# Kernel optimization log

Measured on AMD Instinct MI355X. Metric: run time of the kernel, lower is better.

The kernel has to match this reference:

```python
import jax, jax.numpy as jnp
import numpy as np


def setup_inputs() -> dict:
    key = jax.random.key(0)
    k1, k2, k3 = jax.random.split(key, 3)
    inp = jax.random.normal(k1, (32, 128, 56, 56), dtype=jnp.float32)
    # kaiming-style scale for a 3x3 conv kernel
    fan_in = 128 * 3 * 3
    kernel = jax.random.normal(k2, (256, 128, 3, 3), dtype=jnp.float32) * np.float32(np.sqrt(2.0 / fan_in))
    bias = jax.random.normal(k3, (256,), dtype=jnp.float32)
    return {"inp": inp, "kernel": kernel, "bias": bias}


def reference(inp, kernel, bias):
    # 3x3 conv, stride 1, padding 1 (SAME), NCHW / OIHW layout, plus bias.
    out = jax.lax.conv_general_dilated(
        inp, kernel,
        window_strides=(1, 1),
        padding=((1, 1), (1, 1)),
        dimension_numbers=("NCHW", "OIHW", "NCHW"),
    )
    return out + bias[None, :, None, None]
```

## Files before the change

### kernel.cpp

```cpp
#include <hip/hip_runtime.h>
#include <hip/hip_bf16.h>


#define C_IN   128
#define K_OUT  256
#define HW     56
#define IMG    3136
#define NBATCH 32
#define PW     58
#define KTOT   1152
#define IN_WS_USHORT ((size_t)4*NBATCH*PW*256*8)
#define WT_WS_USHORT ((size_t)12*2*1536*8)

typedef __bf16 bf16x8 __attribute__((ext_vector_type(8)));
typedef float  f32x4  __attribute__((ext_vector_type(4)));
typedef unsigned short ushort8 __attribute__((ext_vector_type(8)));

__device__ inline unsigned short f2bf(float f) {
    unsigned int u = __builtin_bit_cast(unsigned int, f);
    u += ((u >> 16) & 1u) + 0x7FFFu;
    return (unsigned short)(u >> 16);
}

__device__ __forceinline__ void gl2lds16(const unsigned short* g, unsigned short* l) {
    __builtin_amdgcn_global_load_lds(
        (const __attribute__((address_space(1))) unsigned int*)g,
        (__attribute__((address_space(3))) unsigned int*)l, 16, 0, 0);
}

__global__ void prep_input(const float* __restrict__ inp,
                           unsigned short* __restrict__ dst) {
    __shared__ unsigned short tile[C_IN * 57];
    int n = blockIdx.x / PW, py = blockIdx.x % PW;
    ushort8* d8 = (ushort8*)dst;
    const bool border = (py == 0 || py == PW - 1);
    if (!border) {
        const float* src = inp + (size_t)n * C_IN * IMG + (py - 1) * HW;
        for (int i = threadIdx.x; i < C_IN * HW; i += 256) {
            int c = i / HW, x = i - c * HW;
            tile[c * 57 + x] = f2bf(src[c * IMG + x]);
        }
        __syncthreads();
    }
    for (int i = threadIdx.x; i < 1024; i += 256) {
        int cq = i >> 8, rem = i & 255;
        int X = ((rem >> 6) & 3) * 16 + (rem & 15);
        int cc = (rem >> 4) & 3;
        ushort8 v = (ushort8)0;
        if (!border && X >= 1 && X <= HW) {
#pragma unroll
            for (int e = 0; e < 8; ++e)
                v[e] = tile[(cq * 32 + cc * 8 + e) * 57 + (X - 1)];
        }
        d8[((size_t)(cq * NBATCH + n) * PW + py) * 256 + rem] = v;
    }
}

__global__ void prep_weights(const float* __restrict__ w,
                             unsigned short* __restrict__ dst) {
    int idx = blockIdx.x * 256 + threadIdx.x;
    int chunk = idx >> 3, e = idx & 7;
    int p = chunk / 3072, rem = chunk - p * 3072;
    int koh = rem / 1536, rem2 = rem - koh * 1536;
    int s = rem2 / 512, rem3 = rem2 - s * 512;
    int koq = rem3 >> 6, cc = (rem3 >> 4) & 3, kor = rem3 & 15;
    int ko = koh * 128 + koq * 16 + kor;
    int cq = p / 3, r = p - 3 * cq;
    int c = cq * 32 + cc * 8 + e;
    dst[idx] = f2bf(w[(ko * C_IN + c) * 9 + r * 3 + s]);
}

__global__ __launch_bounds__(256, 2) void conv_mfma(
        const unsigned short* __restrict__ In,
        const unsigned short* __restrict__ Wt,
        const float* __restrict__ bias,
        float* __restrict__ out) {
    __shared__ unsigned short smem[40960];

    const int tid = threadIdx.x;
    const int lane = tid & 63, wv = tid >> 6;
    const int l15 = lane & 15, lk = lane >> 4;
    const int koh = blockIdx.x;
    const int by = blockIdx.y;
    const int n = by / 14, rb = (by % 14) * 4;

    const int wkol = (wv & 1) * 64;
    const int wpx  = (wv >> 1) * 112;
    const int albase = (wv & 1) * 4096 + lk * 256 + l15 * 16;

    int yl[7], xp[3][7];
#pragma unroll
    for (int nf = 0; nf < 7; ++nf) {
        int p = wpx + nf * 16 + l15;
        yl[nf] = p / 56;
        int x = p - yl[nf] * 56;
#pragma unroll
        for (int s = 0; s < 3; ++s) {
            int X = x + s;
            xp[s][nf] = ((X >> 4) << 10) + lk * 256 + ((X & 15) << 4);
        }
    }

    f32x4 acc[4][7];
#pragma unroll
    for (int m = 0; m < 4; ++m)
#pragma unroll
        for (int nf = 0; nf < 7; ++nf) acc[m][nf] = (f32x4)0.0f;

#define STAGE_W(PHN) do {                                                   \
    _Pragma("unroll")                                                       \
    for (int li = 0; li < 6; ++li) {                                        \
        int chunk = li * 256 + tid;                                         \
        gl2lds16(Wt + ((size_t)((PHN) * 2 + koh)) * 12288 + chunk * 8,      \
                 &smem[((PHN) & 1) * 12288 + chunk * 8]);                   \
    } } while (0)

#define STAGE_ROW(C_, T_) do {                                              \
    gl2lds16(In + ((size_t)(((C_) * NBATCH + n) * PW + rb + (T_))) * 2048 + tid * 8, \
             &smem[24576 + ((6 * (C_) + (T_)) & 7) * 2048 + tid * 8]);      \
} while (0)

    STAGE_W(0);
    STAGE_ROW(0, 0); STAGE_ROW(0, 1); STAGE_ROW(0, 2); STAGE_ROW(0, 3);

#define PHASE(PH) do {                                                      \
    constexpr int cq_ = (PH) / 3, r_ = (PH) % 3;                            \
    if ((PH) < 11) STAGE_W((PH) + 1);                                       \
    if constexpr (r_ == 0) {                                                \
        if constexpr (cq_ < 3) { STAGE_ROW(cq_ + 1, 0); STAGE_ROW(cq_ + 1, 1); } \
        STAGE_ROW(cq_, 4);                                                  \
    } else if constexpr (r_ == 1) {                                         \
        if constexpr (cq_ < 3) STAGE_ROW(cq_ + 1, 2);                       \
        STAGE_ROW(cq_, 5);                                                  \
    } else {                                                                \
        if constexpr (cq_ < 3) STAGE_ROW(cq_ + 1, 3);                       \
    }                                                                       \
    { constexpr int nIss = ((PH) < 11 ? 6 : 0) +                            \
          (r_ == 0 ? (cq_ < 3 ? 3 : 1) : r_ == 1 ? (cq_ < 3 ? 2 : 1)        \
                                       : (cq_ < 3 ? 1 : 0));                \
      asm volatile("s_waitcnt vmcnt(%0)" :: "i"(nIss) : "memory"); }        \
    __builtin_amdgcn_s_barrier();                                           \
    { const char* wb = (const char*)smem + ((PH) & 1) * 24576;              \
      const char* ib = (const char*)smem + 49152;                           \
      int roff[7];                                                          \
      _Pragma("unroll")                                                     \
      for (int nf = 0; nf < 7; ++nf)                                        \
          roff[nf] = ((6 * cq_ + r_ + yl[nf]) & 7) << 12;                   \
      __builtin_amdgcn_s_setprio(1);                                        \
      _Pragma("unroll")                                                     \
      for (int s = 0; s < 3; ++s) {                                         \
          bf16x8 a[4], b[7];                                                \
          _Pragma("unroll")                                                 \
          for (int m = 0; m < 4; ++m)                                       \
              a[m] = *(const bf16x8*)(wb + albase + s * 8192 + m * 1024);   \
          _Pragma("unroll")                                                 \
          for (int nf = 0; nf < 7; ++nf)                                    \
              b[nf] = *(const bf16x8*)(ib + roff[nf] + xp[s][nf]);          \
          _Pragma("unroll")                                                 \
          for (int m = 0; m < 4; ++m)                                       \
              _Pragma("unroll")                                             \
              for (int nf = 0; nf < 7; ++nf)                                \
                  acc[m][nf] = __builtin_amdgcn_mfma_f32_16x16x32_bf16(     \
                      a[m], b[nf], acc[m][nf], 0, 0, 0);                    \
      }                                                                     \
      __builtin_amdgcn_s_setprio(0);                                        \
    }                                                                       \
    __builtin_amdgcn_s_barrier();                                           \
} while (0)

    PHASE(0);  PHASE(1);  PHASE(2);  PHASE(3);
    PHASE(4);  PHASE(5);  PHASE(6);  PHASE(7);
    PHASE(8);  PHASE(9);  PHASE(10); PHASE(11);

#undef PHASE
#undef STAGE_ROW
#undef STAGE_W

    const int sp0 = rb * 56 + wpx;
#pragma unroll
    for (int m = 0; m < 4; ++m) {
        int kb = koh * 128 + wkol + m * 16 + lk * 4;
        f32x4 bs = *(const f32x4*)(bias + kb);
#pragma unroll
        for (int nf = 0; nf < 7; ++nf) {
            float* ob = out + ((size_t)(n * K_OUT + kb) * IMG) + sp0 + nf * 16 + l15;
#pragma unroll
            for (int j = 0; j < 4; ++j)
                ob[(size_t)j * IMG] = acc[m][nf][j] + bs[j];
        }
    }
}

__global__ void conv_naive(const float* __restrict__ inp,
                           const float* __restrict__ ker,
                           const float* __restrict__ bias,
                           float* __restrict__ out, int total) {
    int o = blockIdx.x * blockDim.x + threadIdx.x;
    if (o >= total) return;
    int x = o % HW, y = (o / HW) % HW, ko = (o / IMG) % K_OUT, n = o / (IMG * K_OUT);
    float acc = bias[ko];
    for (int c = 0; c < C_IN; ++c)
        for (int r = 0; r < 3; ++r) {
            int iy = y + r - 1; if ((unsigned)iy >= HW) continue;
            for (int s = 0; s < 3; ++s) {
                int ix = x + s - 1; if ((unsigned)ix >= HW) continue;
                acc += inp[((n * C_IN + c) * HW + iy) * HW + ix]
                     * ker[((ko * C_IN + c) * 3 + r) * 3 + s];
            }
        }
    out[o] = acc;
}

extern "C" void kernel_launch(void* const* d_in, const int* in_sizes, int n_in,
                              void* d_out, int out_size, void* d_ws, size_t ws_size,
                              hipStream_t stream) {
    const float* inp  = (const float*)d_in[0];
    const float* ker  = (const float*)d_in[1];
    const float* bias = (const float*)d_in[2];
    float* out = (float*)d_out;

    const size_t need = (IN_WS_USHORT + WT_WS_USHORT) * 2;
    if (ws_size < need) {
        int total = NBATCH * K_OUT * IMG;
        conv_naive<<<(total + 255) / 256, 256, 0, stream>>>(inp, ker, bias, out, total);
        return;
    }

    unsigned short* inb = (unsigned short*)d_ws;
    unsigned short* wtb = inb + IN_WS_USHORT;

    prep_input<<<NBATCH * PW, 256, 0, stream>>>(inp, inb);
    prep_weights<<<(int)(WT_WS_USHORT / 256), 256, 0, stream>>>(ker, wtb);

    conv_mfma<<<dim3(2, 448), 256, 0, stream>>>(inb, wtb, bias, out);
}
```

Baseline: 81.15 us.

## Load weight fragments directly into registers and shrink LDS to input rows

Weight panels are no longer staged through LDS. Each lane now loads its A fragments straight from global memory into a double-buffered register array, while LDS holds only a 12-slot ring of input rows. The trailing barrier per phase is dropped, the grid axes are swapped so both output-channel halves of a tile are scheduled far apart, and prep_weights writes eight bf16 values per thread. This removes LDS traffic and footprint for weights and halves the barriers, at the cost of many extra VGPRs (24 bf16x8 vectors) that may hurt occupancy under launch_bounds(256,2), plus a ring-reuse hazard that now depends on the slot count alone.

```diff
diff --git a/kernel.cpp b/kernel.cpp
--- a/kernel.cpp
+++ b/kernel.cpp
@@ -8,7 +8,6 @@
 #define IMG    3136
 #define NBATCH 32
 #define PW     58
-#define KTOT   1152
 #define IN_WS_USHORT ((size_t)4*NBATCH*PW*256*8)
 #define WT_WS_USHORT ((size_t)12*2*1536*8)
 
@@ -58,16 +57,18 @@
 
 __global__ void prep_weights(const float* __restrict__ w,
                              unsigned short* __restrict__ dst) {
-    int idx = blockIdx.x * 256 + threadIdx.x;
-    int chunk = idx >> 3, e = idx & 7;
+    int chunk = blockIdx.x * 256 + threadIdx.x;
     int p = chunk / 3072, rem = chunk - p * 3072;
     int koh = rem / 1536, rem2 = rem - koh * 1536;
     int s = rem2 / 512, rem3 = rem2 - s * 512;
     int koq = rem3 >> 6, cc = (rem3 >> 4) & 3, kor = rem3 & 15;
     int ko = koh * 128 + koq * 16 + kor;
     int cq = p / 3, r = p - 3 * cq;
-    int c = cq * 32 + cc * 8 + e;
-    dst[idx] = f2bf(w[(ko * C_IN + c) * 9 + r * 3 + s]);
+    ushort8 v;
+#pragma unroll
+    for (int e = 0; e < 8; ++e)
+        v[e] = f2bf(w[(ko * C_IN + cq * 32 + cc * 8 + e) * 9 + r * 3 + s]);
+    ((ushort8*)dst)[chunk] = v;
 }
 
 __global__ __launch_bounds__(256, 2) void conv_mfma(
@@ -75,18 +76,18 @@
         const unsigned short* __restrict__ Wt,
         const float* __restrict__ bias,
         float* __restrict__ out) {
-    __shared__ unsigned short smem[40960];
+    __shared__ unsigned short smem[24576];
 
     const int tid = threadIdx.x;
     const int lane = tid & 63, wv = tid >> 6;
     const int l15 = lane & 15, lk = lane >> 4;
-    const int koh = blockIdx.x;
-    const int by = blockIdx.y;
+    const int koh = blockIdx.y;
+    const int by = blockIdx.x;
     const int n = by / 14, rb = (by % 14) * 4;
 
     const int wkol = (wv & 1) * 64;
     const int wpx  = (wv >> 1) * 112;
-    const int albase = (wv & 1) * 4096 + lk * 256 + l15 * 16;
+    const int wlane = (wv & 1) * 2048 + lk * 128 + l15 * 8;
 
     int yl[7], xp[3][7];
 #pragma unroll
@@ -107,52 +108,53 @@
 #pragma unroll
         for (int nf = 0; nf < 7; ++nf) acc[m][nf] = (f32x4)0.0f;
 
-#define STAGE_W(PHN) do {                                                   \
+    bf16x8 wbuf[2][12];
+
+#define LOAD_W(PANEL) do {                                                  \
+    const unsigned short* wp = Wt + ((size_t)((PANEL) * 2 + koh)) * 12288 + wlane; \
     _Pragma("unroll")                                                       \
-    for (int li = 0; li < 6; ++li) {                                        \
-        int chunk = li * 256 + tid;                                         \
-        gl2lds16(Wt + ((size_t)((PHN) * 2 + koh)) * 12288 + chunk * 8,      \
-                 &smem[((PHN) & 1) * 12288 + chunk * 8]);                   \
-    } } while (0)
+    for (int s = 0; s < 3; ++s)                                             \
+        _Pragma("unroll")                                                   \
+        for (int m = 0; m < 4; ++m)                                         \
+            wbuf[(PANEL) & 1][s * 4 + m] =                                  \
+                *(const bf16x8*)(wp + s * 4096 + m * 512);                  \
+} while (0)
 
 #define STAGE_ROW(C_, T_) do {                                              \
     gl2lds16(In + ((size_t)(((C_) * NBATCH + n) * PW + rb + (T_))) * 2048 + tid * 8, \
-             &smem[24576 + ((6 * (C_) + (T_)) & 7) * 2048 + tid * 8]);      \
+             &smem[((6 * (C_) + (T_)) % 12) * 2048 + tid * 8]);             \
 } while (0)
 
-    STAGE_W(0);
+    LOAD_W(0);
     STAGE_ROW(0, 0); STAGE_ROW(0, 1); STAGE_ROW(0, 2); STAGE_ROW(0, 3);
 
 #define PHASE(PH) do {                                                      \
     constexpr int cq_ = (PH) / 3, r_ = (PH) % 3;                            \
-    if ((PH) < 11) STAGE_W((PH) + 1);                                       \
+    if constexpr ((PH) < 11) LOAD_W((PH) + 1);                              \
     if constexpr (r_ == 0) {                                                \
-        if constexpr (cq_ < 3) { STAGE_ROW(cq_ + 1, 0); STAGE_ROW(cq_ + 1, 1); } \
         STAGE_ROW(cq_, 4);                                                  \
+        if constexpr (cq_ < 3) STAGE_ROW(cq_ + 1, 0);                       \
     } else if constexpr (r_ == 1) {                                         \
-        if constexpr (cq_ < 3) STAGE_ROW(cq_ + 1, 2);                       \
         STAGE_ROW(cq_, 5);                                                  \
+        if constexpr (cq_ < 3) STAGE_ROW(cq_ + 1, 1);                       \
     } else {                                                                \
-        if constexpr (cq_ < 3) STAGE_ROW(cq_ + 1, 3);                       \
+        if constexpr (cq_ < 3) { STAGE_ROW(cq_ + 1, 2); STAGE_ROW(cq_ + 1, 3); } \
     }                                                                       \
-    { constexpr int nIss = ((PH) < 11 ? 6 : 0) +                            \
-          (r_ == 0 ? (cq_ < 3 ? 3 : 1) : r_ == 1 ? (cq_ < 3 ? 2 : 1)        \
-                                       : (cq_ < 3 ? 1 : 0));                \
-      asm volatile("s_waitcnt vmcnt(%0)" :: "i"(nIss) : "memory"); }        \
-    __builtin_amdgcn_s_barrier();                                           \
-    { const char* wb = (const char*)smem + ((PH) & 1) * 24576;              \
-      const char* ib = (const char*)smem + 49152;                           \
+    { constexpr int nI = (cq_ < 3) ? 2 : (r_ == 2 ? 0 : 1);                 \
+      constexpr int nW = ((PH) < 11) ? 12 : 0;                              \
+      asm volatile("s_waitcnt vmcnt(%0)" :: "i"(nW + nI) : "memory"); }     \
+    asm volatile("s_barrier" ::: "memory");                                 \
+    { const char* ib = (const char*)smem;                                   \
       int roff[7];                                                          \
       _Pragma("unroll")                                                     \
-      for (int nf = 0; nf < 7; ++nf)                                        \
-          roff[nf] = ((6 * cq_ + r_ + yl[nf]) & 7) << 12;                   \
+      for (int nf = 0; nf < 7; ++nf) {                                      \
+          int t = 6 * cq_ + r_ + yl[nf];                                    \
+          roff[nf] = (t >= 12 ? t - 12 : t) << 12;                          \
+      }                                                                     \
       __builtin_amdgcn_s_setprio(1);                                        \
       _Pragma("unroll")                                                     \
       for (int s = 0; s < 3; ++s) {                                         \
-          bf16x8 a[4], b[7];                                                \
-          _Pragma("unroll")                                                 \
-          for (int m = 0; m < 4; ++m)                                       \
-              a[m] = *(const bf16x8*)(wb + albase + s * 8192 + m * 1024);   \
+          bf16x8 b[7];                                                      \
           _Pragma("unroll")                                                 \
           for (int nf = 0; nf < 7; ++nf)                                    \
               b[nf] = *(const bf16x8*)(ib + roff[nf] + xp[s][nf]);          \
@@ -161,11 +163,10 @@
               _Pragma("unroll")                                             \
               for (int nf = 0; nf < 7; ++nf)                                \
                   acc[m][nf] = __builtin_amdgcn_mfma_f32_16x16x32_bf16(     \
-                      a[m], b[nf], acc[m][nf], 0, 0, 0);                    \
+                      wbuf[(PH) & 1][s * 4 + m], b[nf], acc[m][nf], 0, 0, 0); \
       }                                                                     \
       __builtin_amdgcn_s_setprio(0);                                        \
     }                                                                       \
-    __builtin_amdgcn_s_barrier();                                           \
 } while (0)
 
     PHASE(0);  PHASE(1);  PHASE(2);  PHASE(3);
@@ -174,7 +175,7 @@
 
 #undef PHASE
 #undef STAGE_ROW
-#undef STAGE_W
+#undef LOAD_W
 
     const int sp0 = rb * 56 + wpx;
 #pragma unroll
@@ -230,7 +231,7 @@
     unsigned short* wtb = inb + IN_WS_USHORT;
 
     prep_input<<<NBATCH * PW, 256, 0, stream>>>(inp, inb);
-    prep_weights<<<(int)(WT_WS_USHORT / 256), 256, 0, stream>>>(ker, wtb);
-
-    conv_mfma<<<dim3(2, 448), 256, 0, stream>>>(inb, wtb, bias, out);
-}
+    prep_weights<<<144, 256, 0, stream>>>(ker, wtb);
+
+    conv_mfma<<<dim3(448, 2), 256, 0, stream>>>(inb, wtb, bias, out);
+}
```

New measurement: 118.8 us. +46.4%, slower.
